# Optimization experiments

Hardware: AMD Instinct MI355X
Metric: run time of the kernel (lower is better)

Reference implementation:

```python
import jax, jax.numpy as jnp
import numpy as np


def _gru_cell(x, h, Wih, Whh):
    # PyTorch GRU (bias=False): gates ordered [r, z, n] along rows of W.
    gi = x @ Wih.T              # [B, 3H]
    gh = h @ Whh.T              # [B, 3H]
    ir, iz, inn = jnp.split(gi, 3, axis=-1)
    hr, hz, hn = jnp.split(gh, 3, axis=-1)
    r = jax.nn.sigmoid(ir + hr)
    z = jax.nn.sigmoid(iz + hz)
    n = jnp.tanh(inn + r * hn)
    return (1.0 - z) * n + z * h


def setup_inputs() -> dict:
    key = jax.random.key(0)
    ks = jax.random.split(key, 16)
    B, T = 256, 1024
    U, Z, Y, H = 16, 16, 16, 128
    W = 0.1  # weight scale for stable recurrence
    inp = {
        "u": jax.random.normal(ks[0], (B, U, T), jnp.float32),
        "y": jax.random.normal(ks[1], (B, Y, T), jnp.float32),
        "h0": jax.random.uniform(ks[2], (2, B, H), jnp.float32),
        "Wih0": W * jax.random.normal(ks[3], (3 * H, U + Z), jnp.float32),
        "Whh0": W * jax.random.normal(ks[4], (3 * H, H), jnp.float32),
        "Wih1": W * jax.random.normal(ks[5], (3 * H, H), jnp.float32),
        "Whh1": W * jax.random.normal(ks[6], (3 * H, H), jnp.float32),
        "dW1": W * jax.random.normal(ks[7], (H, U + H), jnp.float32),
        "db1": jnp.zeros((H,), jnp.float32),
        "dW2": W * jax.random.normal(ks[8], (Z, H), jnp.float32),
        "db2": jnp.zeros((Z,), jnp.float32),
        "mW1": W * jax.random.normal(ks[9], (H, Z + H), jnp.float32),
        "mb1": jnp.zeros((H,), jnp.float32),
        "mW2": W * jax.random.normal(ks[10], (H, H), jnp.float32),
        "mb2": jnp.zeros((H,), jnp.float32),
        "mW3": W * jax.random.normal(ks[11], (Y, H), jnp.float32),
        "mb3": jnp.zeros((Y,), jnp.float32),
    }
    return inp


def reference(u, y, h0, Wih0, Whh0, Wih1, Whh1,
              dW1, db1, dW2, db2, mW1, mb1, mW2, mb2, mW3, mb3):
    B, Z = u.shape[0], dW2.shape[0]
    u_t = jnp.transpose(u, (2, 0, 1))  # [T, B, U]
    y_t = jnp.transpose(y, (2, 0, 1))  # [T, B, Y]

    def step(carry, xs):
        h, x_prev, loss = carry  # h: [2, B, H]
        ut, yt = xs
        inp = jnp.concatenate([ut, x_prev], axis=1)       # [B, U+Z]
        h0n = _gru_cell(inp, h[0], Wih0, Whh0)
        h1n = _gru_cell(h0n, h[1], Wih1, Whh1)
        h_new = jnp.stack([h0n, h1n], axis=0)
        # dynn: two Linears, no activation; input cat(u_t, h[-1])
        d_in = jnp.concatenate([ut, h1n], axis=1)         # [B, U+H]
        x_t = (d_in @ dW1.T + db1) @ dW2.T + db2          # [B, Z]
        # menn: Linear -> ReLU -> Linear -> Linear; input cat(x_t, h[0])
        m_in = jnp.concatenate([x_t, h0n], axis=1)        # [B, Z+H]
        m = jax.nn.relu(m_in @ mW1.T + mb1)
        m = m @ mW2.T + mb2
        y_hat = m @ mW3.T + mb3                           # [B, Y]
        loss = loss + jnp.sum((y_hat - yt) ** 2)
        return (h_new, x_t, loss), None

    x0 = jnp.zeros((B, Z), jnp.float32)  # x_tm1 at t=0 is zeros
    (_, _, loss), _ = jax.lax.scan(step, (h0, x0, jnp.float32(0.0)), (u_t, y_t))
    return loss
```

## Files before the change

kernel.cpp:

```cpp
#include <hip/hip_runtime.h>

typedef __bf16 bf16x8 __attribute__((ext_vector_type(8)));
typedef float f32x4 __attribute__((ext_vector_type(4)));
typedef unsigned int uint32;
typedef unsigned short u16;

#define T_STEPS 1024

#define H0_OFF   0
#define H1_OFF   8704
#define M1_OFF   17408
#define UCH_OFF  21760
#define YCH_OFF  46848
#define WL_OFF   71936
#define LDS_BYTES 146688
#define CH_STR   784

#define TG0 0
#define TG1 24
#define TG2 120
#define TG3 216
#define TG4 312
#define TG5 317
#define TG6 357
#define NT_TOT 361
#define SC_DC  369664
#define SC_ME  378880
#define SC_DBC 387072
#define SC_MBE 387136

static __device__ __forceinline__ u16 f2bf(float f) {
    uint32 u = __builtin_bit_cast(uint32, f);
    return (u16)((u + 0x7FFFu + ((u >> 16) & 1u)) >> 16);
}
static __device__ __forceinline__ float bf2f(u16 h) {
    uint32 u = ((uint32)h) << 16;
    return __builtin_bit_cast(float, u);
}
static __device__ __forceinline__ uint32 cvtpk(float a, float b) {
    uint32 r;
    asm("v_cvt_pk_bf16_f32 %0, %1, %2" : "=v"(r) : "v"(a), "v"(b));
    return r;
}
static __device__ __forceinline__ float sigm(float x) {
    return __builtin_amdgcn_rcpf(1.f + __builtin_amdgcn_exp2f(x * -1.4426950408889634f));
}
static __device__ __forceinline__ float tanh_fast(float x) {
    float xm = fmaxf(x, -30.f);
    float e = __builtin_amdgcn_exp2f(xm * -2.8853900817779268f);
    return fmaf(2.f, __builtin_amdgcn_rcpf(e + 1.f), -1.f);
}
static __device__ __forceinline__ f32x4 mfma16(bf16x8 a, bf16x8 b, f32x4 c) {
    return __builtin_amdgcn_mfma_f32_16x16x32_bf16(a, b, c, 0, 0, 0);
}
static __device__ __forceinline__ bf16x8 ldsAF(const char* p) {
    return __builtin_bit_cast(bf16x8, *(const uint4*)p);
}

__global__ void prep1(const float* __restrict__ dW1, const float* __restrict__ db1,
                      const float* __restrict__ dW2, const float* __restrict__ db2,
                      const float* __restrict__ mW2, const float* __restrict__ mb2,
                      const float* __restrict__ mW3, const float* __restrict__ mb3,
                      char* __restrict__ ws, float* __restrict__ out) {
    int id = blockIdx.x * 256 + threadIdx.x;
    if (id == 0) *out = 0.f;
    if (id < 2304) {
        int n = id / 144, k = id % 144;
        float s = 0.f;
        for (int h = 0; h < 128; ++h) s += dW2[n * 128 + h] * dW1[h * 144 + k];
        ((float*)(ws + SC_DC))[id] = s;
    } else if (id < 4352) {
        int e = id - 2304, n = e / 128, k = e % 128;
        float s = 0.f;
        for (int h = 0; h < 128; ++h) s += mW3[n * 128 + h] * mW2[h * 128 + k];
        ((float*)(ws + SC_ME))[e] = s;
    } else if (id < 4368) {
        int n = id - 4352;
        float s = db2[n];
        for (int h = 0; h < 128; ++h) s += dW2[n * 128 + h] * db1[h];
        ((float*)(ws + SC_DBC))[n] = s;
    } else if (id < 4384) {
        int n = id - 4368;
        float s = mb3[n];
        for (int h = 0; h < 128; ++h) s += mW3[n * 128 + h] * mb2[h];
        ((float*)(ws + SC_MBE))[n] = s;
    }
}

__global__ void prep2(const float* __restrict__ W0, const float* __restrict__ W1,
                      const float* __restrict__ W2, const float* __restrict__ W3,
                      const float* __restrict__ W5, char* __restrict__ ws) {
    const int tt = blockIdx.x;
    const int lane = threadIdx.x;
    const int cum[8] = {TG0, TG1, TG2, TG3, TG4, TG5, TG6, NT_TOT};
    const int Kreal[7] = {32, 128, 128, 128, 144, 144, 128};
    const int KT[7] = {1, 4, 4, 4, 5, 5, 4};
    const float* Ws[7] = {W0, W1, W2, W3, (const float*)(ws + SC_DC), W5, (const float*)(ws + SC_ME)};
    int g = 0;
    while (tt >= cum[g + 1]) ++g;
    const int tl = tt - cum[g];
    const int kt = tl % KT[g];
    const int n = (tl / KT[g]) * 16 + (lane & 15);
    const float* W = Ws[g];
    u16* o = (u16*)ws + tt * 512 + lane * 8;
#pragma unroll
    for (int j = 0; j < 8; ++j) {
        int k = kt * 32 + (lane >> 4) * 8 + j;
        o[j] = (k < Kreal[g]) ? f2bf(W[n * Kreal[g] + k]) : (u16)0;
    }
}

__global__ __launch_bounds__(256, 1) void rnn_main(
    const float* __restrict__ u, const float* __restrict__ yg, const float* __restrict__ h0g,
    const char* __restrict__ ws, const float* __restrict__ mb1g,
    const float* __restrict__ dbCg, const float* __restrict__ mbEg,
    float* __restrict__ out) {
    __shared__ __align__(16) char smem[LDS_BYTES];
    const int tid = threadIdx.x;
    const int lane = tid & 63;
    const int w = tid >> 6;
    const int lr = lane & 15;
    const int lg = lane >> 4;
    const int r0 = blockIdx.x * 16;
    const uint4* F4 = (const uint4*)ws;
    const f32x4 zero = {0.f, 0.f, 0.f, 0.f};

    for (int i = tid; i < 1024; i += 256) {
        int lay = i >> 9, rem = i & 511, rr = rem >> 5, k4 = rem & 31;
        float4 v = *(const float4*)(h0g + (lay * 256 + r0 + rr) * 128 + k4 * 4);
        uint2 pk;
        pk.x = (uint32)f2bf(v.x) | ((uint32)f2bf(v.y) << 16);
        pk.y = (uint32)f2bf(v.z) | ((uint32)f2bf(v.w) << 16);
        *(uint2*)(smem + H0_OFF + lay * 8704 + rr * 272 + k4 * 8) = pk;
    }
    for (int i = tid; i < 73 * 64; i += 256) {
        int li = i >> 6, ln2 = i & 63;
        int gt2 = (li < 24) ? li : (li < 29) ? TG4 + (li - 24) : (li < 69) ? TG5 + (li - 29) : TG6 + (li - 69);
        *((uint4*)(smem + WL_OFF) + i) = F4[gt2 * 64 + ln2];
    }
    __syncthreads();

    bf16x8 wW[3][3][2][4];
    for (int p = 0; p < 6; ++p) {
        for (int i = tid; i < 3072; i += 256)
            *((uint4*)(smem + UCH_OFF) + i) = F4[(TG1 + p * 48) * 64 + i];
        __syncthreads();
#pragma unroll
        for (int mat = 0; mat < 3; ++mat)
#pragma unroll
            for (int gg = 0; gg < 3; ++gg)
#pragma unroll
                for (int j = 0; j < 2; ++j) {
                    int rel0 = mat * 96 + gg * 32 + (2 * w + j) * 4;
                    if (rel0 >= p * 48 && rel0 < p * 48 + 48) {
#pragma unroll
                        for (int kt = 0; kt < 4; ++kt)
                            wW[mat][gg][j][kt] =
                                ldsAF(smem + UCH_OFF + (rel0 - p * 48 + kt) * 1024 + lane * 16);
                    }
                }
        __syncthreads();
    }

    float mb1_c[2] = {mb1g[w * 32 + lr], mb1g[w * 32 + 16 + lr]};
    const float mbE_l = mbEg[lr];
    float dbc4[4];
#pragma unroll
    for (int i = 0; i < 4; ++i) dbc4[i] = dbCg[lg * 4 + i];
    float hp0[2][4], hp1[2][4];
#pragma unroll
    for (int j = 0; j < 2; ++j)
#pragma unroll
        for (int i = 0; i < 4; ++i) {
            hp0[j][i] = h0g[(r0 + lg * 4 + i) * 128 + w * 32 + j * 16 + lr];
            hp1[j][i] = h0g[(256 + r0 + lg * 4 + i) * 128 + w * 32 + j * 16 + lr];
        }
    float loss = 0.f;
    const int bp0 = (lr + (lg & 1) * 32) * 4;

    bf16x8 pf_ah[4];
#pragma unroll
    for (int kt = 0; kt < 4; ++kt) pf_ah[kt] = ldsAF(smem + H0_OFF + lr * 272 + kt * 64 + lg * 16);

#pragma unroll 2
    for (int t = 0; t < T_STEPS; ++t) {
        const char* h0c = smem + H0_OFF + (t & 1) * 4352;
        char* h0n = smem + H0_OFF + ((t & 1) ^ 1) * 4352;
        const char* h1c = smem + H1_OFF + (t & 1) * 4352;
        char* h1n = smem + H1_OFF + ((t & 1) ^ 1) * 4352;
        const int s = t & 31, sp = (t - 1) & 31;
        const char* h1r = h1c + lr * 272;

        bf16x8 ad0 = ldsAF((lg < 2) ? (smem + UCH_OFF + sp * CH_STR + lr * 48 + lg * 16)
                                    : (h1r + (lg - 2) * 16));
        bf16x8 ad1 = ldsAF(h1r + 32 + lg * 16);
        bf16x8 ad2 = ldsAF(h1r + 96 + lg * 16);
        bf16x8 ad3 = ldsAF(h1r + 160 + lg * 16);
        bf16x8 ad4 = ldsAF(h1r + 224 + (lg & 1) * 16);
        bf16x8 wd0 = ldsAF(smem + WL_OFF + 24 * 1024 + lane * 16);
        bf16x8 wd1 = ldsAF(smem + WL_OFF + 25 * 1024 + lane * 16);
        bf16x8 wd2 = ldsAF(smem + WL_OFF + 26 * 1024 + lane * 16);
        bf16x8 wd3 = ldsAF(smem + WL_OFF + 27 * 1024 + lane * 16);
        bf16x8 wd4 = ldsAF(smem + WL_OFF + 28 * 1024 + lane * 16);

        f32x4 hR[2], hZ[2], hN[2], nI[2];
#pragma unroll
        for (int j = 0; j < 2; ++j) { hR[j] = zero; hZ[j] = zero; hN[j] = zero; }
#pragma unroll
        for (int kt = 0; kt < 4; ++kt)
#pragma unroll
            for (int j = 0; j < 2; ++j) {
                hR[j] = mfma16(pf_ah[kt], wW[0][0][j][kt], hR[j]);
                hZ[j] = mfma16(pf_ah[kt], wW[0][1][j][kt], hZ[j]);
                hN[j] = mfma16(pf_ah[kt], wW[0][2][j][kt], hN[j]);
            }

        f32x4 xa = mfma16(wd0, ad0, zero);
        xa = mfma16(wd1, ad1, xa);
        xa = mfma16(wd2, ad2, xa);
        f32x4 xb = mfma16(wd3, ad3, zero);
        xb = mfma16(wd4, ad4, xb);
        uint32 pk0 = cvtpk(xa[0] + xb[0] + dbc4[0], xa[1] + xb[1] + dbc4[1]);
        uint32 pk1 = cvtpk(xa[2] + xb[2] + dbc4[2], xa[3] + xb[3] + dbc4[3]);
        if (t == 0) { pk0 = 0u; pk1 = 0u; }
        uint32 d0 = (uint32)__builtin_amdgcn_ds_bpermute(bp0, (int)pk0);
        uint32 d1 = (uint32)__builtin_amdgcn_ds_bpermute(bp0, (int)pk1);
        uint32 d2 = (uint32)__builtin_amdgcn_ds_bpermute(bp0 + 64, (int)pk0);
        uint32 d3 = (uint32)__builtin_amdgcn_ds_bpermute(bp0 + 64, (int)pk1);
        bf16x8 xfrag = __builtin_bit_cast(bf16x8, (uint4){d0, d1, d2, d3});

        if ((t & 31) == 0) {
            __syncthreads();
            for (int q = 0; q < 32; ++q) {
                int pair = w * 64 + q * 2 + (lane >> 5);
                int rr2 = pair >> 4, ch = pair & 15, ss = lane & 31;
                float v = u[(r0 + rr2) * 16384 + ch * 1024 + t + ss];
                *(u16*)(smem + UCH_OFF + ss * CH_STR + rr2 * 48 + ch * 2) = f2bf(v);
                int gt = t - 1 + ss;
                if (gt >= 0) {
                    float vy = yg[(r0 + rr2) * 16384 + ch * 1024 + gt];
                    *(u16*)(smem + YCH_OFF + ss * CH_STR + rr2 * 48 + ch * 2) = f2bf(vy);
                }
            }
            __syncthreads();
        }

        bf16x8 ufrag = ldsAF(smem + UCH_OFF + s * CH_STR + lr * 48 + (lg & 1) * 16);
        bf16x8 a_inp = (lg < 2) ? ufrag : xfrag;
#pragma unroll
        for (int j = 0; j < 2; ++j) {
            bf16x8 b0r = ldsAF(smem + WL_OFF + (0 * 8 + 2 * w + j) * 1024 + lane * 16);
            bf16x8 b0z = ldsAF(smem + WL_OFF + (1 * 8 + 2 * w + j) * 1024 + lane * 16);
            bf16x8 b0n = ldsAF(smem + WL_OFF + (2 * 8 + 2 * w + j) * 1024 + lane * 16);
            hR[j] = mfma16(a_inp, b0r, hR[j]);
            hZ[j] = mfma16(a_inp, b0z, hZ[j]);
            nI[j] = mfma16(a_inp, b0n, zero);
        }
        const char* h0r = h0c + lr * 272;
        bf16x8 am0 = (lg < 2) ? xfrag : ldsAF(h0r + (lg - 2) * 16);
        bf16x8 am1 = ldsAF(h0r + 32 + lg * 16);
        bf16x8 am2 = ldsAF(h0r + 96 + lg * 16);
        bf16x8 am3 = ldsAF(h0r + 160 + lg * 16);
        bf16x8 am4 = ldsAF(h0r + 224 + (lg & 1) * 16);
        f32x4 m[2];
#pragma unroll
        for (int j = 0; j < 2; ++j) {
            const int mb = 29 + (2 * w + j) * 5;
            m[j] = mfma16(am1, ldsAF(smem + WL_OFF + (mb + 1) * 1024 + lane * 16), zero);
            m[j] = mfma16(am2, ldsAF(smem + WL_OFF + (mb + 2) * 1024 + lane * 16), m[j]);
            m[j] = mfma16(am0, ldsAF(smem + WL_OFF + (mb + 0) * 1024 + lane * 16), m[j]);
            m[j] = mfma16(am3, ldsAF(smem + WL_OFF + (mb + 3) * 1024 + lane * 16), m[j]);
            m[j] = mfma16(am4, ldsAF(smem + WL_OFF + (mb + 4) * 1024 + lane * 16), m[j]);
        }
#pragma unroll
        for (int j = 0; j < 2; ++j) {
            const int c2 = (w * 32 + j * 16 + lr) * 2;
#pragma unroll
            for (int i = 0; i < 4; ++i) {
                float rr = sigm(hR[j][i]);
                float zz = sigm(hZ[j][i]);
                float nn = tanh_fast(fmaf(rr, hN[j][i], nI[j][i]));
                float hnew = fmaf(zz, hp0[j][i] - nn, nn);
                hp0[j][i] = hnew;
                *(u16*)(h0n + (lg * 4 + i) * 272 + c2) = (u16)cvtpk(hnew, hnew);
                float mv = fmaxf(m[j][i] + mb1_c[j], 0.f);
                *(u16*)(smem + M1_OFF + (lg * 4 + i) * 272 + c2) = (u16)cvtpk(mv, mv);
            }
        }
        bf16x8 pf_av[4];
#pragma unroll
        for (int kt = 0; kt < 4; ++kt) pf_av[kt] = ldsAF(h1r + kt * 64 + lg * 16);
        __syncthreads();

        const char* h0nr = h0n + lr * 272;
        bf16x8 ag[4];
#pragma unroll
        for (int kt = 0; kt < 4; ++kt) ag[kt] = ldsAF(h0nr + kt * 64 + lg * 16);
        bf16x8 q0, q1, q2, q3, we0, we1, we2, we3;
        if (w == 3) {
            const char* m1r = smem + M1_OFF + lr * 272;
            q0 = ldsAF(m1r + lg * 16);
            q1 = ldsAF(m1r + 64 + lg * 16);
            q2 = ldsAF(m1r + 128 + lg * 16);
            q3 = ldsAF(m1r + 192 + lg * 16);
            we0 = ldsAF(smem + WL_OFF + 69 * 1024 + lane * 16);
            we1 = ldsAF(smem + WL_OFF + 70 * 1024 + lane * 16);
            we2 = ldsAF(smem + WL_OFF + 71 * 1024 + lane * 16);
            we3 = ldsAF(smem + WL_OFF + 72 * 1024 + lane * 16);
        }
        f32x4 R[2], Z[2], Nh[2], Ni[2];
#pragma unroll
        for (int j = 0; j < 2; ++j) { R[j] = zero; Z[j] = zero; Nh[j] = zero; Ni[j] = zero; }
#pragma unroll
        for (int kt = 0; kt < 4; ++kt)
#pragma unroll
            for (int j = 0; j < 2; ++j) {
                R[j] = mfma16(pf_av[kt], wW[2][0][j][kt], R[j]);
                Z[j] = mfma16(pf_av[kt], wW[2][1][j][kt], Z[j]);
                Nh[j] = mfma16(pf_av[kt], wW[2][2][j][kt], Nh[j]);
            }
#pragma unroll
        for (int kt = 0; kt < 4; ++kt)
#pragma unroll
            for (int j = 0; j < 2; ++j) {
                R[j] = mfma16(ag[kt], wW[1][0][j][kt], R[j]);
                Z[j] = mfma16(ag[kt], wW[1][1][j][kt], Z[j]);
                Ni[j] = mfma16(ag[kt], wW[1][2][j][kt], Ni[j]);
            }
        if (w == 3) {
            f32x4 lA = mfma16(q0, we0, zero);
            lA = mfma16(q1, we1, lA);
            f32x4 lB = mfma16(q2, we2, zero);
            lB = mfma16(q3, we3, lB);
            const float gd = (t > 0) ? 1.f : 0.f;
#pragma unroll
            for (int i = 0; i < 4; ++i) {
                float yh = lA[i] + lB[i] + mbE_l;
                float yv = bf2f(*(const u16*)(smem + YCH_OFF + s * CH_STR + (lg * 4 + i) * 48 + lr * 2));
                float d = yh - yv;
                loss = fmaf(gd * d, d, loss);
            }
        }
#pragma unroll
        for (int j = 0; j < 2; ++j) {
            const int c2 = (w * 32 + j * 16 + lr) * 2;
#pragma unroll
            for (int i = 0; i < 4; ++i) {
                float rr = sigm(R[j][i]);
                float zz = sigm(Z[j][i]);
                float nn = tanh_fast(fmaf(rr, Nh[j][i], Ni[j][i]));
                float hnew = fmaf(zz, hp1[j][i] - nn, nn);
                hp1[j][i] = hnew;
                *(u16*)(h1n + (lg * 4 + i) * 272 + c2) = (u16)cvtpk(hnew, hnew);
            }
        }
#pragma unroll
        for (int kt = 0; kt < 4; ++kt) pf_ah[kt] = ag[kt];
        __syncthreads();
    }

    {
        const char* h0c = smem + H0_OFF;
        const char* h1c = smem + H1_OFF;
        const char* h1r = h1c + lr * 272;
        const char* h0r = h0c + lr * 272;
        bf16x8 ad0 = ldsAF((lg < 2) ? (smem + UCH_OFF + 31 * CH_STR + lr * 48 + lg * 16)
                                    : (h1r + (lg - 2) * 16));
        bf16x8 ad1 = ldsAF(h1r + 32 + lg * 16);
        bf16x8 ad2 = ldsAF(h1r + 96 + lg * 16);
        bf16x8 ad3 = ldsAF(h1r + 160 + lg * 16);
        bf16x8 ad4 = ldsAF(h1r + 224 + (lg & 1) * 16);
        f32x4 xa = mfma16(ldsAF(smem + WL_OFF + 24 * 1024 + lane * 16), ad0, zero);
        xa = mfma16(ldsAF(smem + WL_OFF + 25 * 1024 + lane * 16), ad1, xa);
        xa = mfma16(ldsAF(smem + WL_OFF + 26 * 1024 + lane * 16), ad2, xa);
        f32x4 xb = mfma16(ldsAF(smem + WL_OFF + 27 * 1024 + lane * 16), ad3, zero);
        xb = mfma16(ldsAF(smem + WL_OFF + 28 * 1024 + lane * 16), ad4, xb);
        uint32 pk0 = cvtpk(xa[0] + xb[0] + dbc4[0], xa[1] + xb[1] + dbc4[1]);
        uint32 pk1 = cvtpk(xa[2] + xb[2] + dbc4[2], xa[3] + xb[3] + dbc4[3]);
        uint32 d0 = (uint32)__builtin_amdgcn_ds_bpermute(bp0, (int)pk0);
        uint32 d1 = (uint32)__builtin_amdgcn_ds_bpermute(bp0, (int)pk1);
        uint32 d2 = (uint32)__builtin_amdgcn_ds_bpermute(bp0 + 64, (int)pk0);
        uint32 d3 = (uint32)__builtin_amdgcn_ds_bpermute(bp0 + 64, (int)pk1);
        bf16x8 xfrag = __builtin_bit_cast(bf16x8, (uint4){d0, d1, d2, d3});
        bf16x8 am0 = (lg < 2) ? xfrag : ldsAF(h0r + (lg - 2) * 16);
        bf16x8 am1 = ldsAF(h0r + 32 + lg * 16);
        bf16x8 am2 = ldsAF(h0r + 96 + lg * 16);
        bf16x8 am3 = ldsAF(h0r + 160 + lg * 16);
        bf16x8 am4 = ldsAF(h0r + 224 + (lg & 1) * 16);
#pragma unroll
        for (int j = 0; j < 2; ++j) {
            const int mb = 29 + (2 * w + j) * 5;
            f32x4 m = mfma16(am0, ldsAF(smem + WL_OFF + (mb + 0) * 1024 + lane * 16), zero);
            m = mfma16(am1, ldsAF(smem + WL_OFF + (mb + 1) * 1024 + lane * 16), m);
            m = mfma16(am2, ldsAF(smem + WL_OFF + (mb + 2) * 1024 + lane * 16), m);
            m = mfma16(am3, ldsAF(smem + WL_OFF + (mb + 3) * 1024 + lane * 16), m);
            m = mfma16(am4, ldsAF(smem + WL_OFF + (mb + 4) * 1024 + lane * 16), m);
            const int c2 = (w * 32 + j * 16 + lr) * 2;
#pragma unroll
            for (int i = 0; i < 4; ++i) {
                float mv = fmaxf(m[i] + mb1_c[j], 0.f);
                *(u16*)(smem + M1_OFF + (lg * 4 + i) * 272 + c2) = (u16)cvtpk(mv, mv);
            }
        }
        __syncthreads();
        if (w == 3) {
            const char* m1r = smem + M1_OFF + lr * 272;
            bf16x8 q0 = ldsAF(m1r + lg * 16);
            bf16x8 q1 = ldsAF(m1r + 64 + lg * 16);
            bf16x8 q2 = ldsAF(m1r + 128 + lg * 16);
            bf16x8 q3 = ldsAF(m1r + 192 + lg * 16);
            f32x4 lA = mfma16(q0, ldsAF(smem + WL_OFF + 69 * 1024 + lane * 16), zero);
            lA = mfma16(q1, ldsAF(smem + WL_OFF + 70 * 1024 + lane * 16), lA);
            f32x4 lB = mfma16(q2, ldsAF(smem + WL_OFF + 71 * 1024 + lane * 16), zero);
            lB = mfma16(q3, ldsAF(smem + WL_OFF + 72 * 1024 + lane * 16), lB);
#pragma unroll
            for (int i = 0; i < 4; ++i) {
                float yh = lA[i] + lB[i] + mbE_l;
                float yv = yg[(r0 + lg * 4 + i) * 16384 + lr * 1024 + 1023];
                float d = yh - yv;
                loss = fmaf(d, d, loss);
            }
        }
    }

    if (w == 3) {
#pragma unroll
        for (int off = 32; off > 0; off >>= 1) loss += __shfl_down(loss, off, 64);
        if (lane == 0) atomicAdd(out, loss);
    }
}

extern "C" void kernel_launch(void* const* d_in, const int* in_sizes, int n_in,
                              void* d_out, int out_size, void* d_ws, size_t ws_size,
                              hipStream_t stream) {
    const float* u    = (const float*)d_in[0];
    const float* y    = (const float*)d_in[1];
    const float* h0   = (const float*)d_in[2];
    const float* Wih0 = (const float*)d_in[3];
    const float* Whh0 = (const float*)d_in[4];
    const float* Wih1 = (const float*)d_in[5];
    const float* Whh1 = (const float*)d_in[6];
    const float* dW1  = (const float*)d_in[7];
    const float* db1  = (const float*)d_in[8];
    const float* dW2  = (const float*)d_in[9];
    const float* db2  = (const float*)d_in[10];
    const float* mW1  = (const float*)d_in[11];
    const float* mb1  = (const float*)d_in[12];
    const float* mW2  = (const float*)d_in[13];
    const float* mb2  = (const float*)d_in[14];
    const float* mW3  = (const float*)d_in[15];
    const float* mb3  = (const float*)d_in[16];
    float* out = (float*)d_out;
    char* ws = (char*)d_ws;

    prep1<<<dim3(18), dim3(256), 0, stream>>>(dW1, db1, dW2, db2, mW2, mb2, mW3, mb3, ws, out);
    prep2<<<dim3(NT_TOT), dim3(64), 0, stream>>>(Wih0, Whh0, Wih1, Whh1, mW1, ws);
    rnn_main<<<dim3(16), dim3(256), 0, stream>>>(u, y, h0, ws, mb1,
                                                 (const float*)(ws + SC_DBC),
                                                 (const float*)(ws + SC_MBE), out);
}
```

Measured before the change: 3.118 ms.

## Split hidden columns across eight waves instead of four per block

Doubles the block to 512 threads so each wave owns 16 hidden columns instead of 32. This halves the serial MFMA chain and gate math per wave on the latency-bound recurrence. It also keeps the dynn weight fragments in registers instead of reloading them from LDS every step. The u/y chunk loads now pack two channels per 32-bit store. The cost is more waves contending at each per-step barrier, and the launch-bounds change alters the register budget available per thread.

Result: slower. 3.545 ms (+13.7%).

```diff
diff --git a/kernel.cpp b/kernel.cpp
--- a/kernel.cpp
+++ b/kernel.cpp
@@ -6,6 +6,7 @@
 typedef unsigned short u16;
 
 #define T_STEPS 1024
+#define CH_STR 784
 
 #define H0_OFF   0
 #define H1_OFF   8704
@@ -14,7 +15,6 @@
 #define YCH_OFF  46848
 #define WL_OFF   71936
 #define LDS_BYTES 146688
-#define CH_STR   784
 
 #define TG0 0
 #define TG1 24
@@ -110,7 +110,7 @@
     }
 }
 
-__global__ __launch_bounds__(256, 1) void rnn_main(
+__global__ __launch_bounds__(512, 2) void rnn_main(
     const float* __restrict__ u, const float* __restrict__ yg, const float* __restrict__ h0g,
     const char* __restrict__ ws, const float* __restrict__ mb1g,
     const float* __restrict__ dbCg, const float* __restrict__ mbEg,
@@ -125,7 +125,7 @@
     const uint4* F4 = (const uint4*)ws;
     const f32x4 zero = {0.f, 0.f, 0.f, 0.f};
 
-    for (int i = tid; i < 1024; i += 256) {
+    for (int i = tid; i < 1024; i += 512) {
         int lay = i >> 9, rem = i & 511, rr = rem >> 5, k4 = rem & 31;
         float4 v = *(const float4*)(h0g + (lay * 256 + r0 + rr) * 128 + k4 * 4);
         uint2 pk;
@@ -133,49 +133,48 @@
         pk.y = (uint32)f2bf(v.z) | ((uint32)f2bf(v.w) << 16);
         *(uint2*)(smem + H0_OFF + lay * 8704 + rr * 272 + k4 * 8) = pk;
     }
-    for (int i = tid; i < 73 * 64; i += 256) {
+    for (int i = tid; i < 73 * 64; i += 512) {
         int li = i >> 6, ln2 = i & 63;
         int gt2 = (li < 24) ? li : (li < 29) ? TG4 + (li - 24) : (li < 69) ? TG5 + (li - 29) : TG6 + (li - 69);
         *((uint4*)(smem + WL_OFF) + i) = F4[gt2 * 64 + ln2];
     }
     __syncthreads();
 
-    bf16x8 wW[3][3][2][4];
+    bf16x8 wW[3][3][4];
     for (int p = 0; p < 6; ++p) {
-        for (int i = tid; i < 3072; i += 256)
+        for (int i = tid; i < 3072; i += 512)
             *((uint4*)(smem + UCH_OFF) + i) = F4[(TG1 + p * 48) * 64 + i];
         __syncthreads();
 #pragma unroll
         for (int mat = 0; mat < 3; ++mat)
 #pragma unroll
-            for (int gg = 0; gg < 3; ++gg)
-#pragma unroll
-                for (int j = 0; j < 2; ++j) {
-                    int rel0 = mat * 96 + gg * 32 + (2 * w + j) * 4;
-                    if (rel0 >= p * 48 && rel0 < p * 48 + 48) {
-#pragma unroll
-                        for (int kt = 0; kt < 4; ++kt)
-                            wW[mat][gg][j][kt] =
-                                ldsAF(smem + UCH_OFF + (rel0 - p * 48 + kt) * 1024 + lane * 16);
-                    }
+            for (int gg = 0; gg < 3; ++gg) {
+                int rel0 = mat * 96 + gg * 32 + w * 4;
+                if (rel0 >= p * 48 && rel0 < p * 48 + 48) {
+#pragma unroll
+                    for (int kt = 0; kt < 4; ++kt)
+                        wW[mat][gg][kt] = ldsAF(smem + UCH_OFF + (rel0 - p * 48 + kt) * 1024 + lane * 16);
                 }
+            }
         __syncthreads();
     }
-
-    float mb1_c[2] = {mb1g[w * 32 + lr], mb1g[w * 32 + 16 + lr]};
+    bf16x8 wdr[5];
+#pragma unroll
+    for (int k = 0; k < 5; ++k) wdr[k] = ldsAF(smem + WL_OFF + (24 + k) * 1024 + lane * 16);
+
+    const float mb1_c = mb1g[w * 16 + lr];
     const float mbE_l = mbEg[lr];
     float dbc4[4];
 #pragma unroll
     for (int i = 0; i < 4; ++i) dbc4[i] = dbCg[lg * 4 + i];
-    float hp0[2][4], hp1[2][4];
-#pragma unroll
-    for (int j = 0; j < 2; ++j)
-#pragma unroll
-        for (int i = 0; i < 4; ++i) {
-            hp0[j][i] = h0g[(r0 + lg * 4 + i) * 128 + w * 32 + j * 16 + lr];
-            hp1[j][i] = h0g[(256 + r0 + lg * 4 + i) * 128 + w * 32 + j * 16 + lr];
-        }
+    float hp0[4], hp1[4];
+#pragma unroll
+    for (int i = 0; i < 4; ++i) {
+        hp0[i] = h0g[(r0 + lg * 4 + i) * 128 + w * 16 + lr];
+        hp1[i] = h0g[(256 + r0 + lg * 4 + i) * 128 + w * 16 + lr];
+    }
     float loss = 0.f;
+    const int c2 = (w * 16 + lr) * 2;
     const int bp0 = (lr + (lg & 1) * 32) * 4;
 
     bf16x8 pf_ah[4];
@@ -197,29 +196,25 @@
         bf16x8 ad2 = ldsAF(h1r + 96 + lg * 16);
         bf16x8 ad3 = ldsAF(h1r + 160 + lg * 16);
         bf16x8 ad4 = ldsAF(h1r + 224 + (lg & 1) * 16);
-        bf16x8 wd0 = ldsAF(smem + WL_OFF + 24 * 1024 + lane * 16);
-        bf16x8 wd1 = ldsAF(smem + WL_OFF + 25 * 1024 + lane * 16);
-        bf16x8 wd2 = ldsAF(smem + WL_OFF + 26 * 1024 + lane * 16);
-        bf16x8 wd3 = ldsAF(smem + WL_OFF + 27 * 1024 + lane * 16);
-        bf16x8 wd4 = ldsAF(smem + WL_OFF + 28 * 1024 + lane * 16);
-
-        f32x4 hR[2], hZ[2], hN[2], nI[2];
-#pragma unroll
-        for (int j = 0; j < 2; ++j) { hR[j] = zero; hZ[j] = zero; hN[j] = zero; }
-#pragma unroll
-        for (int kt = 0; kt < 4; ++kt)
-#pragma unroll
-            for (int j = 0; j < 2; ++j) {
-                hR[j] = mfma16(pf_ah[kt], wW[0][0][j][kt], hR[j]);
-                hZ[j] = mfma16(pf_ah[kt], wW[0][1][j][kt], hZ[j]);
-                hN[j] = mfma16(pf_ah[kt], wW[0][2][j][kt], hN[j]);
-            }
-
-        f32x4 xa = mfma16(wd0, ad0, zero);
-        xa = mfma16(wd1, ad1, xa);
-        xa = mfma16(wd2, ad2, xa);
-        f32x4 xb = mfma16(wd3, ad3, zero);
-        xb = mfma16(wd4, ad4, xb);
+
+        f32x4 rA = mfma16(pf_ah[0], wW[0][0][0], zero);
+        rA = mfma16(pf_ah[1], wW[0][0][1], rA);
+        f32x4 rB = mfma16(pf_ah[2], wW[0][0][2], zero);
+        rB = mfma16(pf_ah[3], wW[0][0][3], rB);
+        f32x4 zA = mfma16(pf_ah[0], wW[0][1][0], zero);
+        zA = mfma16(pf_ah[1], wW[0][1][1], zA);
+        f32x4 zB = mfma16(pf_ah[2], wW[0][1][2], zero);
+        zB = mfma16(pf_ah[3], wW[0][1][3], zB);
+        f32x4 nA = mfma16(pf_ah[0], wW[0][2][0], zero);
+        nA = mfma16(pf_ah[1], wW[0][2][1], nA);
+        f32x4 nB = mfma16(pf_ah[2], wW[0][2][2], zero);
+        nB = mfma16(pf_ah[3], wW[0][2][3], nB);
+
+        f32x4 xa = mfma16(wdr[0], ad0, zero);
+        xa = mfma16(wdr[1], ad1, xa);
+        xa = mfma16(wdr[2], ad2, xa);
+        f32x4 xb = mfma16(wdr[3], ad3, zero);
+        xb = mfma16(wdr[4], ad4, xb);
         uint32 pk0 = cvtpk(xa[0] + xb[0] + dbc4[0], xa[1] + xb[1] + dbc4[1]);
         uint32 pk1 = cvtpk(xa[2] + xb[2] + dbc4[2], xa[3] + xb[3] + dbc4[3]);
         if (t == 0) { pk0 = 0u; pk1 = 0u; }
@@ -231,61 +226,51 @@
 
         if ((t & 31) == 0) {
             __syncthreads();
-            for (int q = 0; q < 32; ++q) {
-                int pair = w * 64 + q * 2 + (lane >> 5);
-                int rr2 = pair >> 4, ch = pair & 15, ss = lane & 31;
-                float v = u[(r0 + rr2) * 16384 + ch * 1024 + t + ss];
-                *(u16*)(smem + UCH_OFF + ss * CH_STR + rr2 * 48 + ch * 2) = f2bf(v);
+#pragma unroll
+            for (int it = 0; it < 8; ++it) {
+                int g = it * 16 + (tid >> 5);
+                int rr2 = g >> 3, chp = g & 7, ss = lane & 31;
+                const float* up = u + (r0 + rr2) * 16384 + (2 * chp) * 1024 + t + ss;
+                *(uint32*)(smem + UCH_OFF + ss * CH_STR + rr2 * 48 + chp * 4) =
+                    cvtpk(up[0], up[1024]);
                 int gt = t - 1 + ss;
-                if (gt >= 0) {
-                    float vy = yg[(r0 + rr2) * 16384 + ch * 1024 + gt];
-                    *(u16*)(smem + YCH_OFF + ss * CH_STR + rr2 * 48 + ch * 2) = f2bf(vy);
-                }
+                const float* yp = yg + (r0 + rr2) * 16384 + (2 * chp) * 1024 + gt;
+                uint32 py = (gt >= 0) ? cvtpk(yp[0], yp[1024]) : 0u;
+                *(uint32*)(smem + YCH_OFF + ss * CH_STR + rr2 * 48 + chp * 4) = py;
             }
             __syncthreads();
         }
 
         bf16x8 ufrag = ldsAF(smem + UCH_OFF + s * CH_STR + lr * 48 + (lg & 1) * 16);
         bf16x8 a_inp = (lg < 2) ? ufrag : xfrag;
-#pragma unroll
-        for (int j = 0; j < 2; ++j) {
-            bf16x8 b0r = ldsAF(smem + WL_OFF + (0 * 8 + 2 * w + j) * 1024 + lane * 16);
-            bf16x8 b0z = ldsAF(smem + WL_OFF + (1 * 8 + 2 * w + j) * 1024 + lane * 16);
-            bf16x8 b0n = ldsAF(smem + WL_OFF + (2 * 8 + 2 * w + j) * 1024 + lane * 16);
-            hR[j] = mfma16(a_inp, b0r, hR[j]);
-            hZ[j] = mfma16(a_inp, b0z, hZ[j]);
-            nI[j] = mfma16(a_inp, b0n, zero);
-        }
+        bf16x8 b0r = ldsAF(smem + WL_OFF + (0 * 8 + w) * 1024 + lane * 16);
+        bf16x8 b0z = ldsAF(smem + WL_OFF + (1 * 8 + w) * 1024 + lane * 16);
+        bf16x8 b0n = ldsAF(smem + WL_OFF + (2 * 8 + w) * 1024 + lane * 16);
+        rA = mfma16(a_inp, b0r, rA);
+        zA = mfma16(a_inp, b0z, zA);
+        f32x4 nI = mfma16(a_inp, b0n, zero);
         const char* h0r = h0c + lr * 272;
         bf16x8 am0 = (lg < 2) ? xfrag : ldsAF(h0r + (lg - 2) * 16);
         bf16x8 am1 = ldsAF(h0r + 32 + lg * 16);
         bf16x8 am2 = ldsAF(h0r + 96 + lg * 16);
         bf16x8 am3 = ldsAF(h0r + 160 + lg * 16);
         bf16x8 am4 = ldsAF(h0r + 224 + (lg & 1) * 16);
-        f32x4 m[2];
-#pragma unroll
-        for (int j = 0; j < 2; ++j) {
-            const int mb = 29 + (2 * w + j) * 5;
-            m[j] = mfma16(am1, ldsAF(smem + WL_OFF + (mb + 1) * 1024 + lane * 16), zero);
-            m[j] = mfma16(am2, ldsAF(smem + WL_OFF + (mb + 2) * 1024 + lane * 16), m[j]);
-            m[j] = mfma16(am0, ldsAF(smem + WL_OFF + (mb + 0) * 1024 + lane * 16), m[j]);
-            m[j] = mfma16(am3, ldsAF(smem + WL_OFF + (mb + 3) * 1024 + lane * 16), m[j]);
-            m[j] = mfma16(am4, ldsAF(smem + WL_OFF + (mb + 4) * 1024 + lane * 16), m[j]);
-        }
-#pragma unroll
-        for (int j = 0; j < 2; ++j) {
-            const int c2 = (w * 32 + j * 16 + lr) * 2;
-#pragma unroll
-            for (int i = 0; i < 4; ++i) {
-                float rr = sigm(hR[j][i]);
-                float zz = sigm(hZ[j][i]);
-                float nn = tanh_fast(fmaf(rr, hN[j][i], nI[j][i]));
-                float hnew = fmaf(zz, hp0[j][i] - nn, nn);
-                hp0[j][i] = hnew;
-                *(u16*)(h0n + (lg * 4 + i) * 272 + c2) = (u16)cvtpk(hnew, hnew);
-                float mv = fmaxf(m[j][i] + mb1_c[j], 0.f);
-                *(u16*)(smem + M1_OFF + (lg * 4 + i) * 272 + c2) = (u16)cvtpk(mv, mv);
-            }
+        const int mb = 29 + w * 5;
+        f32x4 mA = mfma16(am1, ldsAF(smem + WL_OFF + (mb + 1) * 1024 + lane * 16), zero);
+        mA = mfma16(am2, ldsAF(smem + WL_OFF + (mb + 2) * 1024 + lane * 16), mA);
+        mA = mfma16(am0, ldsAF(smem + WL_OFF + (mb + 0) * 1024 + lane * 16), mA);
+        f32x4 mB = mfma16(am3, ldsAF(smem + WL_OFF + (mb + 3) * 1024 + lane * 16), zero);
+        mB = mfma16(am4, ldsAF(smem + WL_OFF + (mb + 4) * 1024 + lane * 16), mB);
+#pragma unroll
+        for (int i = 0; i < 4; ++i) {
+            float rr = sigm(rA[i] + rB[i]);
+            float zz = sigm(zA[i] + zB[i]);
+            float nn = tanh_fast(fmaf(rr, nA[i] + nB[i], nI[i]));
+            float hnew = fmaf(zz, hp0[i] - nn, nn);
+            hp0[i] = hnew;
+            *(u16*)(h0n + (lg * 4 + i) * 272 + c2) = (u16)cvtpk(hnew, hnew);
+            float mv = fmaxf(mA[i] + mB[i] + mb1_c, 0.f);
+            *(u16*)(smem + M1_OFF + (lg * 4 + i) * 272 + c2) = (u16)cvtpk(mv, mv);
         }
         bf16x8 pf_av[4];
 #pragma unroll
@@ -297,7 +282,7 @@
 #pragma unroll
         for (int kt = 0; kt < 4; ++kt) ag[kt] = ldsAF(h0nr + kt * 64 + lg * 16);
         bf16x8 q0, q1, q2, q3, we0, we1, we2, we3;
-        if (w == 3) {
+        if (w == 7) {
             const char* m1r = smem + M1_OFF + lr * 272;
             q0 = ldsAF(m1r + lg * 16);
             q1 = ldsAF(m1r + 64 + lg * 16);
@@ -308,26 +293,31 @@
             we2 = ldsAF(smem + WL_OFF + 71 * 1024 + lane * 16);
             we3 = ldsAF(smem + WL_OFF + 72 * 1024 + lane * 16);
         }
-        f32x4 R[2], Z[2], Nh[2], Ni[2];
-#pragma unroll
-        for (int j = 0; j < 2; ++j) { R[j] = zero; Z[j] = zero; Nh[j] = zero; Ni[j] = zero; }
-#pragma unroll
-        for (int kt = 0; kt < 4; ++kt)
-#pragma unroll
-            for (int j = 0; j < 2; ++j) {
-                R[j] = mfma16(pf_av[kt], wW[2][0][j][kt], R[j]);
-                Z[j] = mfma16(pf_av[kt], wW[2][1][j][kt], Z[j]);
-                Nh[j] = mfma16(pf_av[kt], wW[2][2][j][kt], Nh[j]);
-            }
-#pragma unroll
-        for (int kt = 0; kt < 4; ++kt)
-#pragma unroll
-            for (int j = 0; j < 2; ++j) {
-                R[j] = mfma16(ag[kt], wW[1][0][j][kt], R[j]);
-                Z[j] = mfma16(ag[kt], wW[1][1][j][kt], Z[j]);
-                Ni[j] = mfma16(ag[kt], wW[1][2][j][kt], Ni[j]);
-            }
-        if (w == 3) {
+        f32x4 bRh = mfma16(pf_av[0], wW[2][0][0], zero);
+        bRh = mfma16(pf_av[1], wW[2][0][1], bRh);
+        bRh = mfma16(pf_av[2], wW[2][0][2], bRh);
+        bRh = mfma16(pf_av[3], wW[2][0][3], bRh);
+        f32x4 bZh = mfma16(pf_av[0], wW[2][1][0], zero);
+        bZh = mfma16(pf_av[1], wW[2][1][1], bZh);
+        bZh = mfma16(pf_av[2], wW[2][1][2], bZh);
+        bZh = mfma16(pf_av[3], wW[2][1][3], bZh);
+        f32x4 bNh = mfma16(pf_av[0], wW[2][2][0], zero);
+        bNh = mfma16(pf_av[1], wW[2][2][1], bNh);
+        bNh = mfma16(pf_av[2], wW[2][2][2], bNh);
+        bNh = mfma16(pf_av[3], wW[2][2][3], bNh);
+        f32x4 bRi = mfma16(ag[0], wW[1][0][0], zero);
+        bRi = mfma16(ag[1], wW[1][0][1], bRi);
+        bRi = mfma16(ag[2], wW[1][0][2], bRi);
+        bRi = mfma16(ag[3], wW[1][0][3], bRi);
+        f32x4 bZi = mfma16(ag[0], wW[1][1][0], zero);
+        bZi = mfma16(ag[1], wW[1][1][1], bZi);
+        bZi = mfma16(ag[2], wW[1][1][2], bZi);
+        bZi = mfma16(ag[3], wW[1][1][3], bZi);
+        f32x4 bNi = mfma16(ag[0], wW[1][2][0], zero);
+        bNi = mfma16(ag[1], wW[1][2][1], bNi);
+        bNi = mfma16(ag[2], wW[1][2][2], bNi);
+        bNi = mfma16(ag[3], wW[1][2][3], bNi);
+        if (w == 7) {
             f32x4 lA = mfma16(q0, we0, zero);
             lA = mfma16(q1, we1, lA);
             f32x4 lB = mfma16(q2, we2, zero);
@@ -342,17 +332,13 @@
             }
         }
 #pragma unroll
-        for (int j = 0; j < 2; ++j) {
-            const int c2 = (w * 32 + j * 16 + lr) * 2;
-#pragma unroll
-            for (int i = 0; i < 4; ++i) {
-                float rr = sigm(R[j][i]);
-                float zz = sigm(Z[j][i]);
-                float nn = tanh_fast(fmaf(rr, Nh[j][i], Ni[j][i]));
-                float hnew = fmaf(zz, hp1[j][i] - nn, nn);
-                hp1[j][i] = hnew;
-                *(u16*)(h1n + (lg * 4 + i) * 272 + c2) = (u16)cvtpk(hnew, hnew);
-            }
+        for (int i = 0; i < 4; ++i) {
+            float rr = sigm(bRi[i] + bRh[i]);
+            float zz = sigm(bZi[i] + bZh[i]);
+            float nn = tanh_fast(fmaf(rr, bNh[i], bNi[i]));
+            float hnew = fmaf(zz, hp1[i] - nn, nn);
+            hp1[i] = hnew;
+            *(u16*)(h1n + (lg * 4 + i) * 272 + c2) = (u16)cvtpk(hnew, hnew);
         }
 #pragma unroll
         for (int kt = 0; kt < 4; ++kt) pf_ah[kt] = ag[kt];
@@ -370,11 +356,11 @@
         bf16x8 ad2 = ldsAF(h1r + 96 + lg * 16);
         bf16x8 ad3 = ldsAF(h1r + 160 + lg * 16);
         bf16x8 ad4 = ldsAF(h1r + 224 + (lg & 1) * 16);
-        f32x4 xa = mfma16(ldsAF(smem + WL_OFF + 24 * 1024 + lane * 16), ad0, zero);
-        xa = mfma16(ldsAF(smem + WL_OFF + 25 * 1024 + lane * 16), ad1, xa);
-        xa = mfma16(ldsAF(smem + WL_OFF + 26 * 1024 + lane * 16), ad2, xa);
-        f32x4 xb = mfma16(ldsAF(smem + WL_OFF + 27 * 1024 + lane * 16), ad3, zero);
-        xb = mfma16(ldsAF(smem + WL_OFF + 28 * 1024 + lane * 16), ad4, xb);
+        f32x4 xa = mfma16(wdr[0], ad0, zero);
+        xa = mfma16(wdr[1], ad1, xa);
+        xa = mfma16(wdr[2], ad2, xa);
+        f32x4 xb = mfma16(wdr[3], ad3, zero);
+        xb = mfma16(wdr[4], ad4, xb);
         uint32 pk0 = cvtpk(xa[0] + xb[0] + dbc4[0], xa[1] + xb[1] + dbc4[1]);
         uint32 pk1 = cvtpk(xa[2] + xb[2] + dbc4[2], xa[3] + xb[3] + dbc4[3]);
         uint32 d0 = (uint32)__builtin_amdgcn_ds_bpermute(bp0, (int)pk0);
@@ -387,23 +373,19 @@
         bf16x8 am2 = ldsAF(h0r + 96 + lg * 16);
         bf16x8 am3 = ldsAF(h0r + 160 + lg * 16);
         bf16x8 am4 = ldsAF(h0r + 224 + (lg & 1) * 16);
-#pragma unroll
-        for (int j = 0; j < 2; ++j) {
-            const int mb = 29 + (2 * w + j) * 5;
-            f32x4 m = mfma16(am0, ldsAF(smem + WL_OFF + (mb + 0) * 1024 + lane * 16), zero);
-            m = mfma16(am1, ldsAF(smem + WL_OFF + (mb + 1) * 1024 + lane * 16), m);
-            m = mfma16(am2, ldsAF(smem + WL_OFF + (mb + 2) * 1024 + lane * 16), m);
-            m = mfma16(am3, ldsAF(smem + WL_OFF + (mb + 3) * 1024 + lane * 16), m);
-            m = mfma16(am4, ldsAF(smem + WL_OFF + (mb + 4) * 1024 + lane * 16), m);
-            const int c2 = (w * 32 + j * 16 + lr) * 2;
-#pragma unroll
-            for (int i = 0; i < 4; ++i) {
-                float mv = fmaxf(m[i] + mb1_c[j], 0.f);
-                *(u16*)(smem + M1_OFF + (lg * 4 + i) * 272 + c2) = (u16)cvtpk(mv, mv);
-            }
+        const int mb = 29 + w * 5;
+        f32x4 m = mfma16(am0, ldsAF(smem + WL_OFF + (mb + 0) * 1024 + lane * 16), zero);
+        m = mfma16(am1, ldsAF(smem + WL_OFF + (mb + 1) * 1024 + lane * 16), m);
+        m = mfma16(am2, ldsAF(smem + WL_OFF + (mb + 2) * 1024 + lane * 16), m);
+        m = mfma16(am3, ldsAF(smem + WL_OFF + (mb + 3) * 1024 + lane * 16), m);
+        m = mfma16(am4, ldsAF(smem + WL_OFF + (mb + 4) * 1024 + lane * 16), m);
+#pragma unroll
+        for (int i = 0; i < 4; ++i) {
+            float mv = fmaxf(m[i] + mb1_c, 0.f);
+            *(u16*)(smem + M1_OFF + (lg * 4 + i) * 272 + c2) = (u16)cvtpk(mv, mv);
         }
         __syncthreads();
-        if (w == 3) {
+        if (w == 7) {
             const char* m1r = smem + M1_OFF + lr * 272;
             bf16x8 q0 = ldsAF(m1r + lg * 16);
             bf16x8 q1 = ldsAF(m1r + 64 + lg * 16);
@@ -423,7 +405,7 @@
         }
     }
 
-    if (w == 3) {
+    if (w == 7) {
 #pragma unroll
         for (int off = 32; off > 0; off >>= 1) loss += __shfl_down(loss, off, 64);
         if (lane == 0) atomicAdd(out, loss);
@@ -455,7 +437,7 @@
 
     prep1<<<dim3(18), dim3(256), 0, stream>>>(dW1, db1, dW2, db2, mW2, mb2, mW3, mb3, ws, out);
     prep2<<<dim3(NT_TOT), dim3(64), 0, stream>>>(Wih0, Whh0, Wih1, Whh1, mW1, ws);
-    rnn_main<<<dim3(16), dim3(256), 0, stream>>>(u, y, h0, ws, mb1,
+    rnn_main<<<dim3(16), dim3(512), 0, stream>>>(u, y, h0, ws, mb1,
                                                  (const float*)(ws + SC_DBC),
                                                  (const float*)(ws + SC_MBE), out);
 }
```
